# Kernel tuning notes

Hardware: AMD Instinct MI355X
Metric: run time of the kernel (lower is better)

The kernel has to match this reference:

```python
import jax, jax.numpy as jnp
import numpy as np

TOP_K = 6
NORM_TOPK_PROB = True


def setup_inputs() -> dict:
    key = jax.random.key(0)
    k1, k2 = jax.random.split(key)
    hidden_states = jax.random.normal(k1, (4, 4096, 2048), dtype=jnp.float32)
    # kaiming_uniform_(a=sqrt(5)) on (E, H): bound = sqrt(6/((1+5)*H)) = 1/sqrt(H)
    bound = 1.0 / np.sqrt(2048)
    weight = jax.random.uniform(k2, (64, 2048), dtype=jnp.float32, minval=-bound, maxval=bound)
    return {"hidden_states": hidden_states, "weight": weight}


def reference(hidden_states, weight):
    bsz, seq_len, h = hidden_states.shape
    x = hidden_states.reshape(-1, h)                      # [T, H]
    logits = jnp.einsum("th,eh->te", x, weight)           # [T, E]
    topk_weight, topk_idx = jax.lax.top_k(logits, TOP_K)  # [T, K]
    topk_weight = jax.nn.softmax(topk_weight, axis=-1)
    if TOP_K > 1 and NORM_TOPK_PROB:
        denom = jnp.sum(topk_weight, axis=-1, keepdims=True) + 1e-20
        topk_weight = topk_weight / denom
    # eval path: aux_loss is None; return routing indices and weights
    return topk_idx, topk_weight
```

## Files before the change

### kernel.cpp

```cpp
#include <hip/hip_runtime.h>
#include <math.h>

#define NTOK 16384
#define HDIM 2048
#define NEXP 64
#define TOPK 6
#define TB   64
#define CH   128
#define NCH  (HDIM / CH)

__device__ __forceinline__ int swz(int row, int h) {
    return row * CH + (h ^ (((row >> 2) & 7) << 2));
}

__global__ __launch_bounds__(256, 1) void moe_gate_kernel(
        const float* __restrict__ x,
        const float* __restrict__ w,
        float* __restrict__ out)
{
    __shared__ float xs[TB * CH];
    __shared__ float ws[NEXP * CH];
    __shared__ float lg[TB * (NEXP + 1)];

    const int tid   = threadIdx.x;
    const int tbase = blockIdx.x * TB;

    const int ge   = tid & 15;
    const int gt   = tid >> 4;
    const int col4 = tid & 31;
    const int row0 = tid >> 5;

    float4 acc[4][4];
    #pragma unroll
    for (int r = 0; r < 4; ++r)
        #pragma unroll
        for (int s = 0; s < 4; ++s)
            acc[r][s] = make_float4(0.f, 0.f, 0.f, 0.f);

    for (int ck = 0; ck < NCH; ++ck) {
        #pragma unroll
        for (int it = 0; it < 8; ++it) {
            const int row = row0 + 8 * it;
            const float4 xv = *(const float4*)&x[(size_t)(tbase + row) * HDIM + ck * CH + 4 * col4];
            *(float4*)&xs[swz(row, 4 * col4)] = xv;
            const float4 wv = *(const float4*)&w[(size_t)row * HDIM + ck * CH + 4 * col4];
            *(float4*)&ws[swz(row, 4 * col4)] = wv;
        }
        __syncthreads();

        #pragma unroll 8
        for (int h0 = 0; h0 < CH; h0 += 4) {
            float4 xv[4], wv[4];
            #pragma unroll
            for (int r = 0; r < 4; ++r)
                xv[r] = *(const float4*)&xs[swz(4 * gt + r, h0)];
            #pragma unroll
            for (int s = 0; s < 4; ++s)
                wv[s] = *(const float4*)&ws[swz(4 * ge + s, h0)];
            #pragma unroll
            for (int r = 0; r < 4; ++r)
                #pragma unroll
                for (int s = 0; s < 4; ++s) {
                    acc[r][s].x = fmaf(xv[r].x, wv[s].x, acc[r][s].x);
                    acc[r][s].y = fmaf(xv[r].y, wv[s].y, acc[r][s].y);
                    acc[r][s].z = fmaf(xv[r].z, wv[s].z, acc[r][s].z);
                    acc[r][s].w = fmaf(xv[r].w, wv[s].w, acc[r][s].w);
                }
        }
        __syncthreads();
    }

    #pragma unroll
    for (int r = 0; r < 4; ++r)
        #pragma unroll
        for (int s = 0; s < 4; ++s) {
            const float4 a = acc[r][s];
            lg[(4 * gt + r) * (NEXP + 1) + (4 * ge + s)] = (a.x + a.z) + (a.y + a.w);
        }
    __syncthreads();

    if (tid < TB) {
        const int tok = tid;
        float val[TOPK];
        int   idx[TOPK];
        #pragma unroll
        for (int k = 0; k < TOPK; ++k) { val[k] = -3.0e38f; idx[k] = 0; }

        for (int e = 0; e < NEXP; ++e) {
            float cv = lg[tok * (NEXP + 1) + e];
            int   ci = e;
            #pragma unroll
            for (int k = 0; k < TOPK; ++k) {
                if (cv > val[k]) {
                    const float tv = val[k]; const int ti = idx[k];
                    val[k] = cv; idx[k] = ci;
                    cv = tv; ci = ti;
                }
            }
        }

        const float m = val[0];
        float ex[TOPK];
        float s = 0.f;
        #pragma unroll
        for (int k = 0; k < TOPK; ++k) { ex[k] = expf(val[k] - m); s += ex[k]; }
        float p[TOPK];
        float d = 0.f;
        #pragma unroll
        for (int k = 0; k < TOPK; ++k) { p[k] = ex[k] / s; d += p[k]; }
        d += 1e-20f;

        const int tg = tbase + tok;
        float* oi = out;
        float* ow = out + (size_t)NTOK * TOPK;
        #pragma unroll
        for (int k = 0; k < TOPK; ++k) {
            oi[tg * TOPK + k] = (float)idx[k];
            ow[tg * TOPK + k] = p[k] / d;
        }
    }
}

extern "C" void kernel_launch(void* const* d_in, const int* in_sizes, int n_in,
                              void* d_out, int out_size, void* d_ws, size_t ws_size,
                              hipStream_t stream) {
    const float* x = (const float*)d_in[0];
    const float* w = (const float*)d_in[1];
    float* out = (float*)d_out;
    dim3 grid(NTOK / TB);
    dim3 block(256);
    hipLaunchKernelGGL(moe_gate_kernel, grid, block, 0, stream, x, w, out);
}
```

Before: 125.0 us.

## Double-buffer smaller tiles with register prefetch and raise occupancy

Shrinks the token tile from 64 to 32 and the hidden chunk from 128 to 64, and double-buffers the shared-memory tiles. The next chunk is prefetched into registers while the current one is computed, so there is one barrier per step. Shared memory is unioned with the logits buffer and launch bounds now allow 4 blocks per CU, giving more blocks and more latency hiding. The cost is less reuse of the weight tile per block: each block re-reads the full weight matrix for only 32 tokens.

Result: slower. 266.1 us (+112.9%).

```diff
diff --git a/kernel.cpp b/kernel.cpp
--- a/kernel.cpp
+++ b/kernel.cpp
@@ -5,77 +5,118 @@
 #define HDIM 2048
 #define NEXP 64
 #define TOPK 6
-#define TB   64
-#define CH   128
-#define NCH  (HDIM / CH)
+#define TB   32
+#define CH   64
+#define NR   (HDIM / CH)
+#define XPAD 68
 
-__device__ __forceinline__ int swz(int row, int h) {
-    return row * CH + (h ^ (((row >> 2) & 7) << 2));
+union SMem {
+    struct {
+        float xs[2][TB][XPAD];
+        float ws[2][NEXP][CH];
+    } s;
+    float lg[TB][NEXP + 1];
+};
+
+__device__ __forceinline__ void load_tiles(const float* __restrict__ x,
+                                           const float* __restrict__ w,
+                                           int tbase, int hbase, int tid,
+                                           float4 xr[2], float4 wr[4]) {
+    #pragma unroll
+    for (int k = 0; k < 2; ++k) {
+        const int f = tid + 256 * k;
+        xr[k] = *(const float4*)&x[(size_t)(tbase + (f >> 4)) * HDIM + hbase + 4 * (f & 15)];
+    }
+    #pragma unroll
+    for (int k = 0; k < 4; ++k) {
+        const int f = tid + 256 * k;
+        wr[k] = *(const float4*)&w[(size_t)(f >> 4) * HDIM + hbase + 4 * (f & 15)];
+    }
 }
 
-__global__ __launch_bounds__(256, 1) void moe_gate_kernel(
+__device__ __forceinline__ void write_tiles(float* xsb, float* wsb, int tid,
+                                            const float4 xr[2], const float4 wr[4]) {
+    #pragma unroll
+    for (int k = 0; k < 2; ++k) {
+        const int f = tid + 256 * k;
+        *(float4*)&xsb[(f >> 4) * XPAD + 4 * (f & 15)] = xr[k];
+    }
+    #pragma unroll
+    for (int k = 0; k < 4; ++k) {
+        const int f = tid + 256 * k;
+        const int row = f >> 4, slot = f & 15;
+        *(float4*)&wsb[row * CH + 4 * (slot ^ ((row >> 2) & 7))] = wr[k];
+    }
+}
+
+#define FMA4(A, X, W)                      \
+    A.x = fmaf(X.x, W.x, A.x);             \
+    A.y = fmaf(X.y, W.y, A.y);             \
+    A.z = fmaf(X.z, W.z, A.z);             \
+    A.w = fmaf(X.w, W.w, A.w);
+
+__global__ __launch_bounds__(256, 4) void moe_gate_kernel(
         const float* __restrict__ x,
         const float* __restrict__ w,
         float* __restrict__ out)
 {
-    __shared__ float xs[TB * CH];
-    __shared__ float ws[NEXP * CH];
-    __shared__ float lg[TB * (NEXP + 1)];
+    __shared__ SMem sm;
 
     const int tid   = threadIdx.x;
+    const int wv    = tid >> 6;
+    const int lane  = tid & 63;
+    const int tokg  = lane >> 4;
+    const int expg  = lane & 15;
+    const int kwb   = (expg & 7) << 4;
     const int tbase = blockIdx.x * TB;
 
-    const int ge   = tid & 15;
-    const int gt   = tid >> 4;
-    const int col4 = tid & 31;
-    const int row0 = tid >> 5;
-
-    float4 acc[4][4];
+    float4 acc[2][4];
     #pragma unroll
-    for (int r = 0; r < 4; ++r)
+    for (int r = 0; r < 2; ++r)
         #pragma unroll
         for (int s = 0; s < 4; ++s)
             acc[r][s] = make_float4(0.f, 0.f, 0.f, 0.f);
 
-    for (int ck = 0; ck < NCH; ++ck) {
-        #pragma unroll
-        for (int it = 0; it < 8; ++it) {
-            const int row = row0 + 8 * it;
-            const float4 xv = *(const float4*)&x[(size_t)(tbase + row) * HDIM + ck * CH + 4 * col4];
-            *(float4*)&xs[swz(row, 4 * col4)] = xv;
-            const float4 wv = *(const float4*)&w[(size_t)row * HDIM + ck * CH + 4 * col4];
-            *(float4*)&ws[swz(row, 4 * col4)] = wv;
+    float4 xr[2], wr[4];
+
+    load_tiles(x, w, tbase, 0, tid, xr, wr);
+    write_tiles(&sm.s.xs[0][0][0], &sm.s.ws[0][0][0], tid, xr, wr);
+    __syncthreads();
+
+    for (int rd = 0; rd < NR; ++rd) {
+        if (rd + 1 < NR) load_tiles(x, w, tbase, (rd + 1) * CH, tid, xr, wr);
+
+        {
+            const int buf = rd & 1;
+            const float* xrow = &sm.s.xs[buf][8 * wv + 2 * tokg][0];
+            const char*  wrow = (const char*)&sm.s.ws[buf][4 * expg][0];
+            #pragma unroll
+            for (int b = 0; b < 16; ++b) {
+                const char* wp = wrow + ((b << 4) ^ kwb);
+                const float4 w0 = *(const float4*)(wp);
+                const float4 w1 = *(const float4*)(wp + CH * 4);
+                const float4 w2 = *(const float4*)(wp + CH * 8);
+                const float4 w3 = *(const float4*)(wp + CH * 12);
+                const float4 x0 = *(const float4*)(xrow + 4 * b);
+                const float4 x1 = *(const float4*)(xrow + XPAD + 4 * b);
+                FMA4(acc[0][0], x0, w0) FMA4(acc[0][1], x0, w1)
+                FMA4(acc[0][2], x0, w2) FMA4(acc[0][3], x0, w3)
+                FMA4(acc[1][0], x1, w0) FMA4(acc[1][1], x1, w1)
+                FMA4(acc[1][2], x1, w2) FMA4(acc[1][3], x1, w3)
+            }
         }
-        __syncthreads();
 
-        #pragma unroll 8
-        for (int h0 = 0; h0 < CH; h0 += 4) {
-            float4 xv[4], wv[4];
-            #pragma unroll
-            for (int r = 0; r < 4; ++r)
-                xv[r] = *(const float4*)&xs[swz(4 * gt + r, h0)];
-            #pragma unroll
-            for (int s = 0; s < 4; ++s)
-                wv[s] = *(const float4*)&ws[swz(4 * ge + s, h0)];
-            #pragma unroll
-            for (int r = 0; r < 4; ++r)
-                #pragma unroll
-                for (int s = 0; s < 4; ++s) {
-                    acc[r][s].x = fmaf(xv[r].x, wv[s].x, acc[r][s].x);
-                    acc[r][s].y = fmaf(xv[r].y, wv[s].y, acc[r][s].y);
-                    acc[r][s].z = fmaf(xv[r].z, wv[s].z, acc[r][s].z);
-                    acc[r][s].w = fmaf(xv[r].w, wv[s].w, acc[r][s].w);
-                }
-        }
+        if (rd + 1 < NR)
+            write_tiles(&sm.s.xs[(rd + 1) & 1][0][0], &sm.s.ws[(rd + 1) & 1][0][0], tid, xr, wr);
         __syncthreads();
     }
 
     #pragma unroll
-    for (int r = 0; r < 4; ++r)
+    for (int r = 0; r < 2; ++r)
         #pragma unroll
         for (int s = 0; s < 4; ++s) {
             const float4 a = acc[r][s];
-            lg[(4 * gt + r) * (NEXP + 1) + (4 * ge + s)] = (a.x + a.z) + (a.y + a.w);
+            sm.lg[8 * wv + 2 * tokg + r][4 * expg + s] = (a.x + a.z) + (a.y + a.w);
         }
     __syncthreads();
 
@@ -87,7 +128,7 @@
         for (int k = 0; k < TOPK; ++k) { val[k] = -3.0e38f; idx[k] = 0; }
 
         for (int e = 0; e < NEXP; ++e) {
-            float cv = lg[tok * (NEXP + 1) + e];
+            float cv = sm.lg[tok][e];
             int   ci = e;
             #pragma unroll
             for (int k = 0; k < TOPK; ++k) {
```

## Shrink token tile, split K across waves, prefetch next chunk into registers

Applied to the files above, without the earlier changes.

Cuts the token tile from 64 to 16 and the block from 256 to 128 threads, giving 1024 blocks instead of 256. Each of the two waves handles half of every 64-wide hidden chunk, and the partial sums are reduced in shared memory before top-k. The weights are stored transposed in shared memory, and the next chunk is prefetched into registers while the current one computes. This aims to fill more CUs and hide global-load latency, at the cost of reloading the whole weight matrix four times as often and doing transposed scalar shared-memory stores.

Result: slower. 200.6 us (+60.4%).

```diff
diff --git a/kernel.cpp b/kernel.cpp
--- a/kernel.cpp
+++ b/kernel.cpp
@@ -5,67 +5,119 @@
 #define HDIM 2048
 #define NEXP 64
 #define TOPK 6
-#define TB   64
-#define CH   128
+#define TB   16
+#define CH   64
 #define NCH  (HDIM / CH)
+#define XPAD 68
 
-__device__ __forceinline__ int swz(int row, int h) {
-    return row * CH + (h ^ (((row >> 2) & 7) << 2));
+union SMem {
+    struct {
+        float wt[CH][NEXP];
+        float xs[TB][XPAD];
+    } s;
+    float lgp[2][TB][4][NEXP];
+};
+
+__device__ __forceinline__ float fcomp(const float4 v, int j) {
+    return j == 0 ? v.x : (j == 1 ? v.y : (j == 2 ? v.z : v.w));
 }
 
-__global__ __launch_bounds__(256, 1) void moe_gate_kernel(
+#define FMA4S(A, S, W)                     \
+    A.x = fmaf(S, W.x, A.x);               \
+    A.y = fmaf(S, W.y, A.y);               \
+    A.z = fmaf(S, W.z, A.z);               \
+    A.w = fmaf(S, W.w, A.w);
+
+__global__ __launch_bounds__(128) void moe_gate_kernel(
         const float* __restrict__ x,
         const float* __restrict__ w,
         float* __restrict__ out)
 {
-    __shared__ float xs[TB * CH];
-    __shared__ float ws[NEXP * CH];
-    __shared__ float lg[TB * (NEXP + 1)];
+    __shared__ SMem sm;
 
     const int tid   = threadIdx.x;
+    const int wv    = tid >> 6;
+    const int lane  = tid & 63;
+    const int q     = lane >> 4;
+    const int eg    = lane & 15;
     const int tbase = blockIdx.x * TB;
 
-    const int ge   = tid & 15;
-    const int gt   = tid >> 4;
-    const int col4 = tid & 31;
-    const int row0 = tid >> 5;
+    const int wr    = tid >> 1;
+    const int whalf = tid & 1;
+    const int xslot = tid & 15;
+    const int xrow  = tid >> 4;
 
     float4 acc[4][4];
     #pragma unroll
     for (int r = 0; r < 4; ++r)
         #pragma unroll
-        for (int s = 0; s < 4; ++s)
-            acc[r][s] = make_float4(0.f, 0.f, 0.f, 0.f);
+        for (int j = 0; j < 4; ++j)
+            acc[r][j] = make_float4(0.f, 0.f, 0.f, 0.f);
+
+    {
+        #pragma unroll
+        for (int m = 0; m < 8; ++m) {
+            const float4 v = *(const float4*)&w[(size_t)wr * HDIM + 4 * (8 * whalf + m)];
+            const int hrow = 4 * (8 * whalf + m);
+            sm.s.wt[hrow + 0][wr] = v.x;
+            sm.s.wt[hrow + 1][wr] = v.y;
+            sm.s.wt[hrow + 2][wr] = v.z;
+            sm.s.wt[hrow + 3][wr] = v.w;
+        }
+        #pragma unroll
+        for (int k = 0; k < 2; ++k) {
+            const float4 v = *(const float4*)&x[(size_t)(tbase + xrow + 8 * k) * HDIM + 4 * xslot];
+            *(float4*)&sm.s.xs[xrow + 8 * k][4 * xslot] = v;
+        }
+    }
+    __syncthreads();
 
     for (int ck = 0; ck < NCH; ++ck) {
+        float4 pw0, pw1, pw2, pw3, pw4, pw5, pw6, pw7, px0, px1;
+        if (ck + 1 < NCH) {
+            const size_t wb = (size_t)wr * HDIM + (size_t)(ck + 1) * CH + 32 * whalf;
+            pw0 = *(const float4*)&w[wb +  0]; pw1 = *(const float4*)&w[wb +  4];
+            pw2 = *(const float4*)&w[wb +  8]; pw3 = *(const float4*)&w[wb + 12];
+            pw4 = *(const float4*)&w[wb + 16]; pw5 = *(const float4*)&w[wb + 20];
+            pw6 = *(const float4*)&w[wb + 24]; pw7 = *(const float4*)&w[wb + 28];
+            px0 = *(const float4*)&x[(size_t)(tbase + xrow) * HDIM + (size_t)(ck + 1) * CH + 4 * xslot];
+            px1 = *(const float4*)&x[(size_t)(tbase + xrow + 8) * HDIM + (size_t)(ck + 1) * CH + 4 * xslot];
+        }
+
         #pragma unroll
-        for (int it = 0; it < 8; ++it) {
-            const int row = row0 + 8 * it;
-            const float4 xv = *(const float4*)&x[(size_t)(tbase + row) * HDIM + ck * CH + 4 * col4];
-            *(float4*)&xs[swz(row, 4 * col4)] = xv;
-            const float4 wv = *(const float4*)&w[(size_t)row * HDIM + ck * CH + 4 * col4];
-            *(float4*)&ws[swz(row, 4 * col4)] = wv;
+        for (int st = 0; st < 8; ++st) {
+            const int h4 = 8 * wv + st;
+            float4 xv[4], wj[4];
+            #pragma unroll
+            for (int r = 0; r < 4; ++r)
+                xv[r] = *(const float4*)&sm.s.xs[4 * q + r][4 * h4];
+            #pragma unroll
+            for (int j = 0; j < 4; ++j)
+                wj[j] = *(const float4*)&sm.s.wt[4 * h4 + j][4 * eg];
+            #pragma unroll
+            for (int r = 0; r < 4; ++r)
+                #pragma unroll
+                for (int j = 0; j < 4; ++j) {
+                    const float sx = fcomp(xv[r], j);
+                    FMA4S(acc[r][j], sx, wj[j])
+                }
         }
         __syncthreads();
 
-        #pragma unroll 8
-        for (int h0 = 0; h0 < CH; h0 += 4) {
-            float4 xv[4], wv[4];
+        if (ck + 1 < NCH) {
+            const int hb0 = 32 * whalf;
             #pragma unroll
-            for (int r = 0; r < 4; ++r)
-                xv[r] = *(const float4*)&xs[swz(4 * gt + r, h0)];
-            #pragma unroll
-            for (int s = 0; s < 4; ++s)
-                wv[s] = *(const float4*)&ws[swz(4 * ge + s, h0)];
-            #pragma unroll
-            for (int r = 0; r < 4; ++r)
-                #pragma unroll
-                for (int s = 0; s < 4; ++s) {
-                    acc[r][s].x = fmaf(xv[r].x, wv[s].x, acc[r][s].x);
-                    acc[r][s].y = fmaf(xv[r].y, wv[s].y, acc[r][s].y);
-                    acc[r][s].z = fmaf(xv[r].z, wv[s].z, acc[r][s].z);
-                    acc[r][s].w = fmaf(xv[r].w, wv[s].w, acc[r][s].w);
-                }
+            for (int m = 0; m < 8; ++m) {
+                const float4 v = (m == 0) ? pw0 : (m == 1) ? pw1 : (m == 2) ? pw2 : (m == 3) ? pw3
+                               : (m == 4) ? pw4 : (m == 5) ? pw5 : (m == 6) ? pw6 : pw7;
+                const int hrow = hb0 + 4 * m;
+                sm.s.wt[hrow + 0][wr] = v.x;
+                sm.s.wt[hrow + 1][wr] = v.y;
+                sm.s.wt[hrow + 2][wr] = v.z;
+                sm.s.wt[hrow + 3][wr] = v.w;
+            }
+            *(float4*)&sm.s.xs[xrow][4 * xslot]     = px0;
+            *(float4*)&sm.s.xs[xrow + 8][4 * xslot] = px1;
         }
         __syncthreads();
     }
@@ -73,21 +125,22 @@
     #pragma unroll
     for (int r = 0; r < 4; ++r)
         #pragma unroll
-        for (int s = 0; s < 4; ++s) {
-            const float4 a = acc[r][s];
-            lg[(4 * gt + r) * (NEXP + 1) + (4 * ge + s)] = (a.x + a.z) + (a.y + a.w);
-        }
+        for (int j = 0; j < 4; ++j)
+            *(float4*)&sm.lgp[wv][4 * q + r][j][4 * eg] = acc[r][j];
     __syncthreads();
 
     if (tid < TB) {
-        const int tok = tid;
         float val[TOPK];
         int   idx[TOPK];
         #pragma unroll
         for (int k = 0; k < TOPK; ++k) { val[k] = -3.0e38f; idx[k] = 0; }
 
         for (int e = 0; e < NEXP; ++e) {
-            float cv = lg[tok * (NEXP + 1) + e];
+            const float J0 = sm.lgp[0][tid][0][e] + sm.lgp[1][tid][0][e];
+            const float J1 = sm.lgp[0][tid][1][e] + sm.lgp[1][tid][1][e];
+            const float J2 = sm.lgp[0][tid][2][e] + sm.lgp[1][tid][2][e];
+            const float J3 = sm.lgp[0][tid][3][e] + sm.lgp[1][tid][3][e];
+            float cv = (J0 + J2) + (J1 + J3);
             int   ci = e;
             #pragma unroll
             for (int k = 0; k < TOPK; ++k) {
@@ -110,7 +163,7 @@
         for (int k = 0; k < TOPK; ++k) { p[k] = ex[k] / s; d += p[k]; }
         d += 1e-20f;
 
-        const int tg = tbase + tok;
+        const int tg = tbase + tid;
         float* oi = out;
         float* ow = out + (size_t)NTOK * TOPK;
         #pragma unroll
@@ -128,6 +181,6 @@
     const float* w = (const float*)d_in[1];
     float* out = (float*)d_out;
     dim3 grid(NTOK / TB);
-    dim3 block(256);
+    dim3 block(128);
     hipLaunchKernelGGL(moe_gate_kernel, grid, block, 0, stream, x, w, out);
 }
```

## Restructure gate GEMM: lane-per-expert, direct x loads, async weight LDS staging

Applied to the files above, without the earlier changes.

Reworks the logits GEMM so each lane owns one expert and each wave handles 8 tokens over half of the hidden dimension. Activations are now read straight from global memory as wave-uniform broadcast loads, and only the weight tile goes through LDS via global_load_lds. Blocks shrink to 32 tokens with 512 threads and target higher occupancy, and the two hidden-dim halves are combined in LDS before top-k. This drops x staging through shared memory and raises parallelism, but relies on scalar or broadcast x loads being efficient. Weight tiles are reloaded for every 32 tokens, which roughly doubles weight traffic.

After: 126.2 us. Within noise of the previous version (+1.0%).

```diff
diff --git a/kernel.cpp b/kernel.cpp
--- a/kernel.cpp
+++ b/kernel.cpp
@@ -1,93 +1,106 @@
 #include <hip/hip_runtime.h>
 #include <math.h>
 
-#define NTOK 16384
-#define HDIM 2048
-#define NEXP 64
-#define TOPK 6
-#define TB   64
-#define CH   128
-#define NCH  (HDIM / CH)
+#define NTOK  16384
+#define HDIM  2048
+#define NEXP  64
+#define TOPK  6
+#define TB    32
+#define CH    64
+#define NCH   16
+#define HHALF 1024
 
-__device__ __forceinline__ int swz(int row, int h) {
-    return row * CH + (h ^ (((row >> 2) & 7) << 2));
+union SMem {
+    float4 wt[2][16][NEXP];
+    struct {
+        float4 cmb[4][8][NEXP];
+        float  lg[TB][65];
+    } e;
+};
+
+__device__ __forceinline__ void gload_lds16(const float* g, void* l) {
+    __builtin_amdgcn_global_load_lds(
+        (const __attribute__((address_space(1))) unsigned int*)g,
+        (__attribute__((address_space(3))) unsigned int*)l, 16, 0, 0);
 }
 
-__global__ __launch_bounds__(256, 1) void moe_gate_kernel(
+__global__ __launch_bounds__(512, 4) void moe_gate_kernel(
         const float* __restrict__ x,
         const float* __restrict__ w,
         float* __restrict__ out)
 {
-    __shared__ float xs[TB * CH];
-    __shared__ float ws[NEXP * CH];
-    __shared__ float lg[TB * (NEXP + 1)];
+    __shared__ SMem sm;
 
-    const int tid   = threadIdx.x;
+    const int tid  = threadIdx.x;
+    const int lane = tid & 63;
+    const int wv   = __builtin_amdgcn_readfirstlane(tid >> 6);
+    const int tg   = wv >> 1;
+    const int hh   = wv & 1;
     const int tbase = blockIdx.x * TB;
 
-    const int ge   = tid & 15;
-    const int gt   = tid >> 4;
-    const int col4 = tid & 31;
-    const int row0 = tid >> 5;
+    const float* xw = x + (size_t)(tbase + tg * 8) * HDIM + hh * HHALF;
 
-    float4 acc[4][4];
+    float4 acc[8];
     #pragma unroll
-    for (int r = 0; r < 4; ++r)
+    for (int t = 0; t < 8; ++t) acc[t] = make_float4(0.f, 0.f, 0.f, 0.f);
+
+    for (int c = 0; c < NCH; ++c) {
+        __syncthreads();
+
         #pragma unroll
-        for (int s = 0; s < 4; ++s)
-            acc[r][s] = make_float4(0.f, 0.f, 0.f, 0.f);
-
-    for (int ck = 0; ck < NCH; ++ck) {
-        #pragma unroll
-        for (int it = 0; it < 8; ++it) {
-            const int row = row0 + 8 * it;
-            const float4 xv = *(const float4*)&x[(size_t)(tbase + row) * HDIM + ck * CH + 4 * col4];
-            *(float4*)&xs[swz(row, 4 * col4)] = xv;
-            const float4 wv = *(const float4*)&w[(size_t)row * HDIM + ck * CH + 4 * col4];
-            *(float4*)&ws[swz(row, 4 * col4)] = wv;
+        for (int k = 0; k < 8; ++k) {
+            const int p  = wv * 8 + k;
+            const int sh = p >> 4;
+            const int sl = p & 15;
+            const float* g = w + (size_t)lane * HDIM + sh * HHALF + c * CH + 4 * sl;
+            gload_lds16(g, &sm.wt[sh][sl][0]);
         }
         __syncthreads();
 
-        #pragma unroll 8
-        for (int h0 = 0; h0 < CH; h0 += 4) {
-            float4 xv[4], wv[4];
+        const float* xc = xw + c * CH;
+        #pragma unroll
+        for (int s = 0; s < 16; ++s) {
+            const float4 wv4 = sm.wt[hh][s][lane];
             #pragma unroll
-            for (int r = 0; r < 4; ++r)
-                xv[r] = *(const float4*)&xs[swz(4 * gt + r, h0)];
-            #pragma unroll
-            for (int s = 0; s < 4; ++s)
-                wv[s] = *(const float4*)&ws[swz(4 * ge + s, h0)];
-            #pragma unroll
-            for (int r = 0; r < 4; ++r)
-                #pragma unroll
-                for (int s = 0; s < 4; ++s) {
-                    acc[r][s].x = fmaf(xv[r].x, wv[s].x, acc[r][s].x);
-                    acc[r][s].y = fmaf(xv[r].y, wv[s].y, acc[r][s].y);
-                    acc[r][s].z = fmaf(xv[r].z, wv[s].z, acc[r][s].z);
-                    acc[r][s].w = fmaf(xv[r].w, wv[s].w, acc[r][s].w);
-                }
+            for (int t = 0; t < 8; ++t) {
+                const float4 xv = *(const float4*)(xc + t * HDIM + 4 * s);
+                acc[t].x = fmaf(xv.x, wv4.x, acc[t].x);
+                acc[t].y = fmaf(xv.y, wv4.y, acc[t].y);
+                acc[t].z = fmaf(xv.z, wv4.z, acc[t].z);
+                acc[t].w = fmaf(xv.w, wv4.w, acc[t].w);
+            }
         }
-        __syncthreads();
     }
 
-    #pragma unroll
-    for (int r = 0; r < 4; ++r)
+    __syncthreads();
+
+    if (hh == 1) {
         #pragma unroll
-        for (int s = 0; s < 4; ++s) {
-            const float4 a = acc[r][s];
-            lg[(4 * gt + r) * (NEXP + 1) + (4 * ge + s)] = (a.x + a.z) + (a.y + a.w);
+        for (int t = 0; t < 8; ++t)
+            sm.e.cmb[tg][t][lane] = acc[t];
+    }
+    __syncthreads();
+    if (hh == 0) {
+        #pragma unroll
+        for (int t = 0; t < 8; ++t) {
+            const float4 o  = sm.e.cmb[tg][t][lane];
+            const float  J0 = acc[t].x + o.x;
+            const float  J1 = acc[t].y + o.y;
+            const float  J2 = acc[t].z + o.z;
+            const float  J3 = acc[t].w + o.w;
+            sm.e.lg[tg * 8 + t][lane] = (J0 + J2) + (J1 + J3);
         }
+    }
     __syncthreads();
 
     if (tid < TB) {
-        const int tok = tid;
         float val[TOPK];
         int   idx[TOPK];
         #pragma unroll
         for (int k = 0; k < TOPK; ++k) { val[k] = -3.0e38f; idx[k] = 0; }
 
         for (int e = 0; e < NEXP; ++e) {
-            float cv = lg[tok * (NEXP + 1) + e];
+            float cv = sm.e.lg[tid][e];
             int   ci = e;
             #pragma unroll
             for (int k = 0; k < TOPK; ++k) {
@@ -110,13 +123,13 @@
         for (int k = 0; k < TOPK; ++k) { p[k] = ex[k] / s; d += p[k]; }
         d += 1e-20f;
 
-        const int tg = tbase + tok;
+        const int tg2 = tbase + tid;
         float* oi = out;
         float* ow = out + (size_t)NTOK * TOPK;
         #pragma unroll
         for (int k = 0; k < TOPK; ++k) {
-            oi[tg * TOPK + k] = (float)idx[k];
-            ow[tg * TOPK + k] = p[k] / d;
+            oi[tg2 * TOPK + k] = (float)idx[k];
+            ow[tg2 * TOPK + k] = p[k] / d;
         }
     }
 }
@@ -128,6 +141,6 @@
     const float* w = (const float*)d_in[1];
     float* out = (float*)d_out;
     dim3 grid(NTOK / TB);
-    dim3 block(256);
+    dim3 block(512);
     hipLaunchKernelGGL(moe_gate_kernel, grid, block, 0, stream, x, w, out);
 }
```
